# Kernel tuning notes

Measured on AMD Instinct MI355X. Metric: run time of the kernel, lower is better.

## Reference

```python
import jax, jax.numpy as jnp
import numpy as np

B = 16384          # batch
F = 64             # number of feature columns (tables)
L = 10             # pooled lookups per feature (bag size)
E = 16             # embedding dim
V = 1_000_000      # hashed vocab size (shared table)
D = F * E          # concat width = 1024
EPS = 1e-5


def setup_inputs() -> dict:
    key = jax.random.key(0)
    ks = jax.random.split(key, 9)
    idx = jax.random.randint(ks[0], (B, F, L), 0, V, dtype=jnp.int64)
    # NormalTensorInitializer(var=0.01) -> std 0.1
    emb = jax.random.normal(ks[1], (V, E), dtype=jnp.float32) * 0.1
    W1 = jax.random.normal(ks[2], (D, 1024), dtype=jnp.float32) / np.sqrt(D).astype(np.float32)
    b1 = jnp.zeros((1024,), jnp.float32)
    W2 = jax.random.normal(ks[3], (1024, 512), dtype=jnp.float32) / np.sqrt(1024).astype(np.float32)
    b2 = jnp.zeros((512,), jnp.float32)
    W3 = jax.random.normal(ks[4], (512, 1), dtype=jnp.float32) / np.sqrt(512).astype(np.float32)
    b3 = jnp.zeros((1,), jnp.float32)
    return {"idx": idx, "emb": emb, "W1": W1, "b1": b1,
            "W2": W2, "b2": b2, "W3": W3, "b3": b3}


def reference(idx, emb, W1, b1, W2, b2, W3, b3):
    # EmbeddingSumConcat: gather [B,F,L,E], sum-pool over bag dim, concat features
    pooled = jnp.take(emb, idx, axis=0).sum(axis=2)          # [B, F, E]
    x = pooled.reshape(B, D)                                  # [B, F*E]
    # ms.nn.Normalization: per-feature batch standardization
    mu = x.mean(axis=0, keepdims=True)
    var = x.var(axis=0, keepdims=True)
    x = (x - mu) * jax.lax.rsqrt(var + EPS)
    # Dense tower 1024 -> 1024 -> 512 -> 1, sigmoid
    h = jax.nn.relu(x @ W1 + b1)
    h = jax.nn.relu(h @ W2 + b2)
    out = jax.nn.sigmoid(h @ W3 + b3)                         # [B, 1]
    return out
```

## Files before the change

kernel.cpp:

```cpp
#include <hip/hip_runtime.h>
#include <hip/hip_bf16.h>
#include <math.h>

typedef __attribute__((ext_vector_type(8))) short  short8;
typedef __attribute__((ext_vector_type(4))) float  f32x4;
typedef __attribute__((ext_vector_type(4))) unsigned short u16x4;
typedef __attribute__((ext_vector_type(8))) unsigned short u16x8;

#define BATCH 16384
#define NF    64
#define BAGL  10
#define ED    16
#define DW    1024
#define VOCAB 1000000

static __device__ __forceinline__ unsigned short f2bf(float f) {
    unsigned int u = __builtin_bit_cast(unsigned int, f);
    unsigned int r = (u + 0x7fffu + ((u >> 16) & 1u)) >> 16;
    return (unsigned short)r;
}
static __device__ __forceinline__ float bf2f(unsigned short h) {
    unsigned int u = ((unsigned int)h) << 16;
    return __builtin_bit_cast(float, u);
}

__global__ __launch_bounds__(256) void emb_to_bf16(const float* __restrict__ e,
                                                   unsigned short* __restrict__ o) {
    const long long i = ((long long)blockIdx.x * 256 + threadIdx.x) * 8;
    if (i >= (long long)VOCAB * ED) return;
    const f32x4 a = *(const f32x4*)(e + i);
    const f32x4 b = *(const f32x4*)(e + i + 4);
    u16x8 r;
#pragma unroll
    for (int j = 0; j < 4; ++j) { r[j] = f2bf(a[j]); r[4 + j] = f2bf(b[j]); }
    *(u16x8*)(o + i) = r;
}

__global__ __launch_bounds__(256) void pool_bf16(const int* __restrict__ idx,
                                                 const unsigned short* __restrict__ embb,
                                                 unsigned short* __restrict__ xb) {
    const int gid = blockIdx.x * 256 + threadIdx.x;
    const int bag = gid >> 1;
    const int h   = gid & 1;
    const int* ip = idx + (long long)bag * BAGL;

    int v[BAGL];
#pragma unroll
    for (int l = 0; l < BAGL; ++l) v[l] = ip[l];
    u16x8 e[BAGL];
#pragma unroll
    for (int l = 0; l < BAGL; ++l)
        e[l] = *(const u16x8*)(embb + (((long long)v[l]) << 4) + h * 8);

    float s[8] = {0, 0, 0, 0, 0, 0, 0, 0};
#pragma unroll
    for (int l = 0; l < BAGL; ++l)
#pragma unroll
        for (int j = 0; j < 8; ++j) s[j] += bf2f(e[l][j]);

    u16x8 o;
#pragma unroll
    for (int j = 0; j < 8; ++j) o[j] = f2bf(s[j]);
    *(u16x8*)(xb + (((long long)bag) << 4) + h * 8) = o;
}

__global__ __launch_bounds__(256) void stats_kernel(const unsigned short* __restrict__ xb,
                                                    float* __restrict__ ssum,
                                                    float* __restrict__ ssq) {
    const int t = threadIdx.x;
    const long long r0 = (long long)blockIdx.x * 128;
    float s[4] = {0, 0, 0, 0}, q[4] = {0, 0, 0, 0};
    for (int r = 0; r < 128; ++r) {
        const u16x4 v = *(const u16x4*)(xb + (r0 + r) * DW + t * 4);
#pragma unroll
        for (int j = 0; j < 4; ++j) { float f = bf2f(v[j]); s[j] += f; q[j] += f * f; }
    }
#pragma unroll
    for (int j = 0; j < 4; ++j) {
        atomicAdd(&ssum[t * 4 + j], s[j]);
        atomicAdd(&ssq [t * 4 + j], q[j]);
    }
}

__global__ void finalize_stats(const float* __restrict__ ssum, const float* __restrict__ ssq,
                               float* __restrict__ mean, float* __restrict__ rsig,
                               float* __restrict__ murs) {
    const int c = blockIdx.x * 256 + threadIdx.x;
    const float m = ssum[c] * (1.0f / (float)BATCH);
    const float v = ssq[c] * (1.0f / (float)BATCH) - m * m;
    const float r = rsqrtf(v + 1e-5f);
    mean[c] = m; rsig[c] = r; murs[c] = m * r;
}

template <int SCALE>
__global__ __launch_bounds__(256) void transpose_f32_bf16(const float* __restrict__ src,
                                                          unsigned short* __restrict__ dst,
                                                          int R, int C,
                                                          const float* __restrict__ rs) {
    __shared__ float tile[32][33];
    const int tx = threadIdx.x & 31, ty = threadIdx.x >> 5;
    const int bx = blockIdx.x, by = blockIdx.y;
#pragma unroll
    for (int i = 0; i < 4; ++i) {
        const int r = by * 32 + ty + i * 8, c = bx * 32 + tx;
        float v = src[(long long)r * C + c];
        if (SCALE) v *= rs[r];
        tile[ty + i * 8][tx] = v;
    }
    __syncthreads();
#pragma unroll
    for (int i = 0; i < 4; ++i) {
        const int oc = bx * 32 + ty + i * 8;
        dst[(long long)oc * R + by * 32 + tx] = f2bf(tile[tx][ty + i * 8]);
    }
}

__global__ __launch_bounds__(256) void b1fold_kernel(const float* __restrict__ W1,
                                                     const float* __restrict__ murs,
                                                     float* __restrict__ b1n) {
    const int n = blockIdx.x * 256 + threadIdx.x;
    const int k0 = blockIdx.y * 128;
    float acc = 0.f;
#pragma unroll 4
    for (int k = 0; k < 128; ++k)
        acc += murs[k0 + k] * W1[(long long)(k0 + k) * 1024 + n];
    atomicAdd(&b1n[n], -acc);
}

#define GEMM_STAGE(dstA, dstB, kt)                                              \
  {                                                                             \
    const int k0s = (kt) * 64;                                                  \
    _Pragma("unroll")                                                           \
    for (int g = 0; g < 4; ++g) {                                               \
      const int cid = g * 256 + tid;                                            \
      const int rr = cid >> 3, pos = cid & 7;                                   \
      const int csrc = (pos ^ (rr & 7)) << 3;                                   \
      __builtin_amdgcn_global_load_lds(                                         \
        (const __attribute__((address_space(1))) void*)(A + a_base + (long long)rr * K + k0s + csrc), \
        (__attribute__((address_space(3))) void*)(&(dstA)[cid * 8]), 16, 0, 0); \
      __builtin_amdgcn_global_load_lds(                                         \
        (const __attribute__((address_space(1))) void*)(Bt + b_base + (long long)rr * K + k0s + csrc), \
        (__attribute__((address_space(3))) void*)(&(dstB)[cid * 8]), 16, 0, 0); \
    }                                                                           \
  }

#define GEMM_CORE_LOOP                                                          \
    const int tid = threadIdx.x;                                                \
    const int w = tid >> 6, l = tid & 63;                                       \
    const int wr = w >> 1, wc = w & 1;                                          \
    const int l15 = l & 15, l4 = l >> 4;                                        \
    f32x4 acc[4][4] = {};                                                       \
    const long long a_base = (long long)bm * 128 * K;                           \
    const long long b_base = (long long)bn * 128 * K;                           \
    const int NT = K >> 6;                                                      \
    GEMM_STAGE(As[0], Bs[0], 0)                                                 \
    GEMM_STAGE(As[1], Bs[1], 1)                                                 \
    asm volatile("s_waitcnt vmcnt(8)" ::: "memory");                            \
    __builtin_amdgcn_sched_barrier(0);                                          \
    __builtin_amdgcn_s_barrier();                                               \
    for (int t = 0; t < NT; ++t) {                                              \
        const unsigned short* Ap = As[t & 1];                                   \
        const unsigned short* Bp = Bs[t & 1];                                   \
        short8 a[2][4], b[2][4];                                                \
        _Pragma("unroll")                                                       \
        for (int kk = 0; kk < 2; ++kk) {                                        \
            const int swz = ((kk * 4 + l4) ^ (l15 & 7)) << 3;                   \
            _Pragma("unroll")                                                   \
            for (int m = 0; m < 4; ++m)                                         \
                a[kk][m] = *(const short8*)(Ap + (wr * 64 + m * 16 + l15) * 64 + swz); \
            _Pragma("unroll")                                                   \
            for (int n = 0; n < 4; ++n)                                         \
                b[kk][n] = *(const short8*)(Bp + (wc * 64 + n * 16 + l15) * 64 + swz); \
        }                                                                       \
        asm volatile("s_waitcnt lgkmcnt(0)" ::: "memory");                      \
        __builtin_amdgcn_sched_barrier(0);                                      \
        __builtin_amdgcn_s_barrier();                                           \
        if (t + 2 < NT) { GEMM_STAGE(As[t & 1], Bs[t & 1], t + 2) }             \
        __builtin_amdgcn_s_setprio(1);                                          \
        _Pragma("unroll")                                                       \
        for (int kk = 0; kk < 2; ++kk)                                          \
            _Pragma("unroll")                                                   \
            for (int m = 0; m < 4; ++m)                                         \
                _Pragma("unroll")                                               \
                for (int n = 0; n < 4; ++n)                                     \
                    acc[m][n] = __builtin_amdgcn_mfma_f32_16x16x32_bf16(        \
                        a[kk][m], b[kk][n], acc[m][n], 0, 0, 0);                \
        __builtin_amdgcn_s_setprio(0);                                          \
        if (t + 1 < NT) {                                                       \
            if (t + 2 < NT) { asm volatile("s_waitcnt vmcnt(8)" ::: "memory"); }\
            else            { asm volatile("s_waitcnt vmcnt(0)" ::: "memory"); }\
            __builtin_amdgcn_sched_barrier(0);                                  \
            __builtin_amdgcn_s_barrier();                                       \
        }                                                                       \
    }

__global__ __launch_bounds__(256, 2) void gemm_relu(const unsigned short* __restrict__ A,
                                                    const unsigned short* __restrict__ Bt,
                                                    const float* __restrict__ bias,
                                                    const float* __restrict__ bias2,
                                                    unsigned short* __restrict__ C,
                                                    int M, int N, int K, int NBN) {
    __shared__ __align__(16) unsigned short As[2][128 * 64];
    __shared__ __align__(16) unsigned short Bs[2][128 * 64];
    const int blk = blockIdx.x, xcd = blk & 7, j = blk >> 3;
    const int bm = xcd * 16 + j / NBN, bn = j % NBN;

    GEMM_CORE_LOOP

#pragma unroll
    for (int m = 0; m < 4; ++m) {
        const int grow_base = bm * 128 + wr * 64 + m * 16 + l4 * 4;
#pragma unroll
        for (int n = 0; n < 4; ++n) {
            const int gcol = bn * 128 + wc * 64 + n * 16 + l15;
            const float bv = bias[gcol] + bias2[gcol];
#pragma unroll
            for (int j2 = 0; j2 < 4; ++j2) {
                float v = fmaxf(acc[m][n][j2] + bv, 0.f);
                C[(long long)(grow_base + j2) * N + gcol] = f2bf(v);
            }
        }
    }
}

__global__ __launch_bounds__(256, 2) void gemm2_fused(const unsigned short* __restrict__ A,
                                                      const unsigned short* __restrict__ Bt,
                                                      const float* __restrict__ bias,
                                                      const float* __restrict__ W3,
                                                      float* __restrict__ logits,
                                                      int M, int N, int K, int NBN) {
    __shared__ __align__(16) unsigned short As[2][128 * 64];
    __shared__ __align__(16) unsigned short Bs[2][128 * 64];
    const int blk = blockIdx.x, xcd = blk & 7, j = blk >> 3;
    const int bm = xcd * 16 + j / NBN, bn = j % NBN;

    GEMM_CORE_LOOP

#pragma unroll
    for (int m = 0; m < 4; ++m) {
        float part[4] = {0.f, 0.f, 0.f, 0.f};
#pragma unroll
        for (int n = 0; n < 4; ++n) {
            const int gcol = bn * 128 + wc * 64 + n * 16 + l15;
            const float bv = bias[gcol];
            const float w3 = W3[gcol];
#pragma unroll
            for (int j2 = 0; j2 < 4; ++j2) {
                float v = fmaxf(acc[m][n][j2] + bv, 0.f);
                part[j2] += v * w3;
            }
        }
#pragma unroll
        for (int off = 1; off < 16; off <<= 1)
#pragma unroll
            for (int j2 = 0; j2 < 4; ++j2) part[j2] += __shfl_xor(part[j2], off, 64);
        if (l15 == 0) {
            const int grow = bm * 128 + wr * 64 + m * 16 + l4 * 4;
#pragma unroll
            for (int j2 = 0; j2 < 4; ++j2) atomicAdd(&logits[grow + j2], part[j2]);
        }
    }
}

__global__ __launch_bounds__(256) void sigmoid_kernel(const float* __restrict__ logits,
                                                      const float* __restrict__ b3,
                                                      float* __restrict__ out) {
    const int i = blockIdx.x * 256 + threadIdx.x;
    out[i] = 1.0f / (1.0f + expf(-(logits[i] + b3[0])));
}

extern "C" void kernel_launch(void* const* d_in, const int* in_sizes, int n_in,
                              void* d_out, int out_size, void* d_ws, size_t ws_size,
                              hipStream_t stream) {
    const int*   idx = (const int*)d_in[0];
    const float* emb = (const float*)d_in[1];
    const float* W1  = (const float*)d_in[2];
    const float* b1  = (const float*)d_in[3];
    const float* W2  = (const float*)d_in[4];
    const float* b2  = (const float*)d_in[5];
    const float* W3  = (const float*)d_in[6];
    const float* b3  = (const float*)d_in[7];
    float* out = (float*)d_out;

    const size_t EMBB_H1_BYTES = (size_t)BATCH * DW * 2;

    char* ws = (char*)d_ws;
    unsigned short* xb   = (unsigned short*)ws; ws += (size_t)BATCH * DW * 2;
    unsigned short* embb = (unsigned short*)ws; ws += EMBB_H1_BYTES;
    unsigned short* h1   = embb;
    unsigned short* w1t  = (unsigned short*)ws; ws += (size_t)1024 * 1024 * 2;
    unsigned short* w2t  = (unsigned short*)ws; ws += (size_t)512 * 1024 * 2;
    float* ssum   = (float*)ws; ws += 4096;
    float* ssq    = (float*)ws; ws += 4096;
    float* b1n    = (float*)ws; ws += 4096;
    float* logits = (float*)ws; ws += (size_t)BATCH * 4;
    float* mean   = (float*)ws; ws += 4096;
    float* rsig   = (float*)ws; ws += 4096;
    float* murs   = (float*)ws; ws += 4096;

    hipMemsetAsync(ssum, 0, 4096 * 3 + (size_t)BATCH * 4, stream);

    const long long embElems = (long long)VOCAB * ED;
    const int embBlocks = (int)((embElems / 8 + 255) / 256);
    emb_to_bf16<<<embBlocks, 256, 0, stream>>>(emb, embb);
    pool_bf16<<<(BATCH * NF * 2) / 256, 256, 0, stream>>>(idx, embb, xb);
    stats_kernel<<<BATCH / 128, 256, 0, stream>>>(xb, ssum, ssq);
    finalize_stats<<<4, 256, 0, stream>>>(ssum, ssq, mean, rsig, murs);

    transpose_f32_bf16<1><<<dim3(32, 32), 256, 0, stream>>>(W1, w1t, 1024, 1024, rsig);
    b1fold_kernel<<<dim3(4, 8), 256, 0, stream>>>(W1, murs, b1n);
    transpose_f32_bf16<0><<<dim3(16, 32), 256, 0, stream>>>(W2, w2t, 1024, 512, nullptr);

    gemm_relu<<<(BATCH / 128) * (1024 / 128), 256, 0, stream>>>(
        xb, w1t, b1, b1n, h1, BATCH, 1024, 1024, 1024 / 128);
    gemm2_fused<<<(BATCH / 128) * (512 / 128), 256, 0, stream>>>(
        h1, w2t, b2, W3, logits, BATCH, 512, 1024, 512 / 128);

    sigmoid_kernel<<<BATCH / 256, 256, 0, stream>>>(logits, b3, out);
}
```

Baseline: 295.5 us.

## Gather fp32 embeddings directly, drop table conversion, fuse weight prep kernels

```diff
diff --git a/kernel.cpp b/kernel.cpp
--- a/kernel.cpp
+++ b/kernel.cpp
@@ -24,53 +24,39 @@
     return __builtin_bit_cast(float, u);
 }
 
-__global__ __launch_bounds__(256) void emb_to_bf16(const float* __restrict__ e,
-                                                   unsigned short* __restrict__ o) {
-    const long long i = ((long long)blockIdx.x * 256 + threadIdx.x) * 8;
-    if (i >= (long long)VOCAB * ED) return;
-    const f32x4 a = *(const f32x4*)(e + i);
-    const f32x4 b = *(const f32x4*)(e + i + 4);
-    u16x8 r;
-#pragma unroll
-    for (int j = 0; j < 4; ++j) { r[j] = f2bf(a[j]); r[4 + j] = f2bf(b[j]); }
-    *(u16x8*)(o + i) = r;
-}
-
-__global__ __launch_bounds__(256) void pool_bf16(const int* __restrict__ idx,
-                                                 const unsigned short* __restrict__ embb,
-                                                 unsigned short* __restrict__ xb) {
+__global__ __launch_bounds__(256) void pool_kernel(const int* __restrict__ idx,
+                                                   const float* __restrict__ emb,
+                                                   unsigned short* __restrict__ xb) {
     const int gid = blockIdx.x * 256 + threadIdx.x;
-    const int bag = gid >> 1;
-    const int h   = gid & 1;
+    const int bag = gid >> 2;
+    const int q   = gid & 3;
     const int* ip = idx + (long long)bag * BAGL;
 
     int v[BAGL];
 #pragma unroll
     for (int l = 0; l < BAGL; ++l) v[l] = ip[l];
-    u16x8 e[BAGL];
+    f32x4 e[BAGL];
 #pragma unroll
     for (int l = 0; l < BAGL; ++l)
-        e[l] = *(const u16x8*)(embb + (((long long)v[l]) << 4) + h * 8);
-
-    float s[8] = {0, 0, 0, 0, 0, 0, 0, 0};
-#pragma unroll
-    for (int l = 0; l < BAGL; ++l)
-#pragma unroll
-        for (int j = 0; j < 8; ++j) s[j] += bf2f(e[l][j]);
-
-    u16x8 o;
-#pragma unroll
-    for (int j = 0; j < 8; ++j) o[j] = f2bf(s[j]);
-    *(u16x8*)(xb + (((long long)bag) << 4) + h * 8) = o;
+        e[l] = *(const f32x4*)(emb + (((long long)v[l]) << 4) + (q << 2));
+
+    f32x4 s01 = e[0] + e[1], s23 = e[2] + e[3], s45 = e[4] + e[5],
+          s67 = e[6] + e[7], s89 = e[8] + e[9];
+    f32x4 acc = ((s01 + s23) + (s45 + s67)) + s89;
+
+    u16x4 o;
+#pragma unroll
+    for (int j = 0; j < 4; ++j) o[j] = f2bf(acc[j]);
+    *(u16x4*)(xb + (((long long)bag) << 4) + (q << 2)) = o;
 }
 
 __global__ __launch_bounds__(256) void stats_kernel(const unsigned short* __restrict__ xb,
                                                     float* __restrict__ ssum,
                                                     float* __restrict__ ssq) {
     const int t = threadIdx.x;
-    const long long r0 = (long long)blockIdx.x * 128;
+    const long long r0 = (long long)blockIdx.x * 8;
     float s[4] = {0, 0, 0, 0}, q[4] = {0, 0, 0, 0};
-    for (int r = 0; r < 128; ++r) {
+    for (int r = 0; r < 8; ++r) {
         const u16x4 v = *(const u16x4*)(xb + (r0 + r) * DW + t * 4);
 #pragma unroll
         for (int j = 0; j < 4; ++j) { float f = bf2f(v[j]); s[j] += f; q[j] += f * f; }
@@ -82,49 +68,57 @@
     }
 }
 
-__global__ void finalize_stats(const float* __restrict__ ssum, const float* __restrict__ ssq,
-                               float* __restrict__ mean, float* __restrict__ rsig,
-                               float* __restrict__ murs) {
-    const int c = blockIdx.x * 256 + threadIdx.x;
+static __device__ __forceinline__ float rsig_of(const float* ssum, const float* ssq, int c) {
     const float m = ssum[c] * (1.0f / (float)BATCH);
     const float v = ssq[c] * (1.0f / (float)BATCH) - m * m;
-    const float r = rsqrtf(v + 1e-5f);
-    mean[c] = m; rsig[c] = r; murs[c] = m * r;
-}
-
-template <int SCALE>
-__global__ __launch_bounds__(256) void transpose_f32_bf16(const float* __restrict__ src,
-                                                          unsigned short* __restrict__ dst,
-                                                          int R, int C,
-                                                          const float* __restrict__ rs) {
+    return rsqrtf(v + 1e-5f);
+}
+
+__global__ __launch_bounds__(256) void prep_weights(const float* __restrict__ W1,
+                                                    const float* __restrict__ W2,
+                                                    const float* __restrict__ ssum,
+                                                    const float* __restrict__ ssq,
+                                                    unsigned short* __restrict__ w1t,
+                                                    unsigned short* __restrict__ w2t,
+                                                    float* __restrict__ b1n) {
+    const int z = blockIdx.z;
+    const int bx = blockIdx.x, by = blockIdx.y;
+    if (z == 2) {
+        if (bx >= 4 || by >= 8) return;
+        __shared__ float mu_s[128];
+        const int n = bx * 256 + threadIdx.x;
+        const int k0 = by * 128;
+        if (threadIdx.x < 128) {
+            const int k = k0 + threadIdx.x;
+            mu_s[threadIdx.x] = ssum[k] * (1.0f / (float)BATCH) * rsig_of(ssum, ssq, k);
+        }
+        __syncthreads();
+        float acc = 0.f;
+#pragma unroll 4
+        for (int k = 0; k < 128; ++k)
+            acc += mu_s[k] * W1[(long long)(k0 + k) * 1024 + n];
+        atomicAdd(&b1n[n], -acc);
+        return;
+    }
+    if (z == 1 && bx >= 16) return;
     __shared__ float tile[32][33];
     const int tx = threadIdx.x & 31, ty = threadIdx.x >> 5;
-    const int bx = blockIdx.x, by = blockIdx.y;
+    const float* src = z ? W2 : W1;
+    unsigned short* dst = z ? w2t : w1t;
+    const int C = z ? 512 : 1024;
 #pragma unroll
     for (int i = 0; i < 4; ++i) {
         const int r = by * 32 + ty + i * 8, c = bx * 32 + tx;
         float v = src[(long long)r * C + c];
-        if (SCALE) v *= rs[r];
+        if (!z) v *= rsig_of(ssum, ssq, r);
         tile[ty + i * 8][tx] = v;
     }
     __syncthreads();
 #pragma unroll
     for (int i = 0; i < 4; ++i) {
         const int oc = bx * 32 + ty + i * 8;
-        dst[(long long)oc * R + by * 32 + tx] = f2bf(tile[tx][ty + i * 8]);
-    }
-}
-
-__global__ __launch_bounds__(256) void b1fold_kernel(const float* __restrict__ W1,
-                                                     const float* __restrict__ murs,
-                                                     float* __restrict__ b1n) {
-    const int n = blockIdx.x * 256 + threadIdx.x;
-    const int k0 = blockIdx.y * 128;
-    float acc = 0.f;
-#pragma unroll 4
-    for (int k = 0; k < 128; ++k)
-        acc += murs[k0 + k] * W1[(long long)(k0 + k) * 1024 + n];
-    atomicAdd(&b1n[n], -acc);
+        dst[(long long)oc * 1024 + by * 32 + tx] = f2bf(tile[tx][ty + i * 8]);
+    }
 }
 
 #define GEMM_STAGE(dstA, dstB, kt)                                              \
@@ -184,7 +178,7 @@
                 _Pragma("unroll")                                               \
                 for (int n = 0; n < 4; ++n)                                     \
                     acc[m][n] = __builtin_amdgcn_mfma_f32_16x16x32_bf16(        \
-                        a[kk][m], b[kk][n], acc[m][n], 0, 0, 0);                \
+                        a[kk][m], b[kk][n], acc[kk ? m : m][n], 0, 0, 0);       \
         __builtin_amdgcn_s_setprio(0);                                          \
         if (t + 1 < NT) {                                                       \
             if (t + 2 < NT) { asm volatile("s_waitcnt vmcnt(8)" ::: "memory"); }\
@@ -282,34 +276,22 @@
     const float* b3  = (const float*)d_in[7];
     float* out = (float*)d_out;
 
-    const size_t EMBB_H1_BYTES = (size_t)BATCH * DW * 2;
-
     char* ws = (char*)d_ws;
     unsigned short* xb   = (unsigned short*)ws; ws += (size_t)BATCH * DW * 2;
-    unsigned short* embb = (unsigned short*)ws; ws += EMBB_H1_BYTES;
-    unsigned short* h1   = embb;
+    unsigned short* h1   = (unsigned short*)ws; ws += (size_t)BATCH * DW * 2;
     unsigned short* w1t  = (unsigned short*)ws; ws += (size_t)1024 * 1024 * 2;
     unsigned short* w2t  = (unsigned short*)ws; ws += (size_t)512 * 1024 * 2;
     float* ssum   = (float*)ws; ws += 4096;
     float* ssq    = (float*)ws; ws += 4096;
     float* b1n    = (float*)ws; ws += 4096;
     float* logits = (float*)ws; ws += (size_t)BATCH * 4;
-    float* mean   = (float*)ws; ws += 4096;
-    float* rsig   = (float*)ws; ws += 4096;
-    float* murs   = (float*)ws; ws += 4096;
 
     hipMemsetAsync(ssum, 0, 4096 * 3 + (size_t)BATCH * 4, stream);
 
-    const long long embElems = (long long)VOCAB * ED;
-    const int embBlocks = (int)((embElems / 8 + 255) / 256);
-    emb_to_bf16<<<embBlocks, 256, 0, stream>>>(emb, embb);
-    pool_bf16<<<(BATCH * NF * 2) / 256, 256, 0, stream>>>(idx, embb, xb);
-    stats_kernel<<<BATCH / 128, 256, 0, stream>>>(xb, ssum, ssq);
-    finalize_stats<<<4, 256, 0, stream>>>(ssum, ssq, mean, rsig, murs);
-
-    transpose_f32_bf16<1><<<dim3(32, 32), 256, 0, stream>>>(W1, w1t, 1024, 1024, rsig);
-    b1fold_kernel<<<dim3(4, 8), 256, 0, stream>>>(W1, murs, b1n);
-    transpose_f32_bf16<0><<<dim3(16, 32), 256, 0, stream>>>(W2, w2t, 1024, 512, nullptr);
+    pool_kernel<<<(BATCH * NF * 4) / 256, 256, 0, stream>>>(idx, emb, xb);
+    stats_kernel<<<BATCH / 8, 256, 0, stream>>>(xb, ssum, ssq);
+
+    prep_weights<<<dim3(32, 32, 3), 256, 0, stream>>>(W1, W2, ssum, ssq, w1t, w2t, b1n);
 
     gemm_relu<<<(BATCH / 128) * (1024 / 128), 256, 0, stream>>>(
         xb, w1t, b1, b1n, h1, BATCH, 1024, 1024, 1024 / 128);
```

New measurement: 474.9 us. 60.7% more time.
